# Optimization experiments

Hardware: AMD Instinct MI355X
Metric: run time of the kernel (lower is better)

Reference implementation:

```python
import jax, jax.numpy as jnp
import numpy as np

N_HEAD = 16
R = 4  # reciprocal rank

def setup_inputs() -> dict:
    key = jax.random.key(0)
    ks = jax.random.split(key, 8)
    B, T, C = 2, 2048, 1024
    H = N_HEAD
    D = C // H
    D_std = D - R
    x = jax.random.normal(ks[0], (B, T, C), dtype=jnp.float32)
    W_attn = jax.random.normal(ks[1], (3 * C, C), dtype=jnp.float32) * (1.0 / np.sqrt(C))
    W_proj = jax.random.normal(ks[2], (C, C), dtype=jnp.float32) * (1.0 / np.sqrt(C))
    w_std = jnp.full((H,), D_std / D, dtype=jnp.float32)
    w_rec = jnp.full((H,), R / D, dtype=jnp.float32)
    skip_std = jnp.float32(2.0)
    skip_low = jnp.float32(-3.0)
    rwr_alpha = jnp.full((H,), 0.05, dtype=jnp.float32)
    return {"x": x, "W_attn": W_attn, "W_proj": W_proj, "w_std": w_std,
            "w_rec": w_rec, "skip_std": skip_std, "skip_low": skip_low,
            "rwr_alpha": rwr_alpha}

def reference(x, W_attn, W_proj, w_std, w_rec, skip_std, skip_low, rwr_alpha):
    B, T, C = x.shape
    H = N_HEAD
    D = C // H
    D_std = D - R
    # fused QKV projection: [Qf | Kf | V]
    fused = jnp.einsum('btc,fc->btf', x, W_attn)
    qf, kf, v = jnp.split(fused, 3, axis=-1)
    Qf = qf.reshape(B, T, H, D).transpose(0, 2, 1, 3)  # (B,H,T,D)
    Kf = kf.reshape(B, T, H, D).transpose(0, 2, 1, 3)
    V = v.reshape(B, T, H, D).transpose(0, 2, 1, 3)
    # dynamic per-head gate scaling folded into Qf/Kf
    g_std = jnp.sqrt(jnp.clip(w_std * jax.nn.sigmoid(skip_std), 1e-8))  # (H,)
    g_rec = jnp.sqrt(jnp.clip(w_rec * jax.nn.sigmoid(skip_low), 1e-8))  # (H,)
    scale = jnp.concatenate([
        jnp.broadcast_to(g_std[:, None], (H, D_std)),
        jnp.broadcast_to(g_rec[:, None], (H, R)),
    ], axis=-1)  # (H, D)
    scale = scale[None, :, None, :]  # (1,H,1,D)
    Qf = Qf * scale
    Kf = Kf * scale
    # causal SDPA (scale = 1/sqrt(head_dim), dropout=0)
    scores = jnp.einsum('bhqd,bhkd->bhqk', Qf, Kf) / jnp.sqrt(jnp.float32(D))
    causal = jnp.tril(jnp.ones((T, T), dtype=bool))
    scores = jnp.where(causal[None, None], scores, jnp.float32(-1e30))
    attn = jax.nn.softmax(scores, axis=-1)
    y = jnp.einsum('bhqk,bhkd->bhqd', attn, V)
    # self-restart mix: out = (1-alpha)*attn_out + alpha*V, alpha in [0, 0.5]
    alpha = jnp.clip(rwr_alpha, 0.0, 0.5)[None, :, None, None]
    y = (1.0 - alpha) * y + alpha * V
    y = y.transpose(0, 2, 1, 3).reshape(B, T, C)
    return jnp.einsum('btc,oc->bto', y, W_proj)
```

## Files before the change

### kernel.cpp

```cpp
#include <hip/hip_runtime.h>
#include <hip/hip_bf16.h>
#include <math.h>
#include <stdint.h>

#define B_    2
#define T_    2048
#define C_    1024
#define H_    16
#define D_    64
#define R_    4
#define DSTD  60
#define F_    3072
#define BT_   (B_ * T_)

typedef __bf16 bf16x8 __attribute__((ext_vector_type(8)));
typedef __bf16 bf16x4 __attribute__((ext_vector_type(4)));
typedef float  f32x4  __attribute__((ext_vector_type(4)));

__device__ __forceinline__ int swz_blk(int row, int blk) {
    return blk ^ ((row >> 1) & 7);
}

__device__ __forceinline__ void gload_lds16(const void* g, void* l) {
    __builtin_amdgcn_global_load_lds(
        (const __attribute__((address_space(1))) uint32_t*)g,
        (__attribute__((address_space(3))) uint32_t*)l, 16, 0, 0);
}

__global__ __launch_bounds__(256) void cast_kernel(
    const float* __restrict__ in, __bf16* __restrict__ outp, int n4)
{
    int i = blockIdx.x * 256 + threadIdx.x;
    if (i < n4) {
        float4 v = ((const float4*)in)[i];
        bf16x4 o;
        o[0] = (__bf16)v.x; o[1] = (__bf16)v.y;
        o[2] = (__bf16)v.z; o[3] = (__bf16)v.w;
        ((bf16x4*)outp)[i] = o;
    }
}

__global__ __launch_bounds__(256) void gemm_qkv_kernel(
    const __bf16* __restrict__ A,
    const __bf16* __restrict__ Bw,
    const float* __restrict__ w_std, const float* __restrict__ w_rec,
    const float* __restrict__ skip_std, const float* __restrict__ skip_low,
    __bf16* __restrict__ Q, __bf16* __restrict__ K, __bf16* __restrict__ V)
{
    __shared__ __bf16 As[128 * 32];
    __shared__ __bf16 Bs[128 * 32];

    const int tid  = threadIdx.x;
    const int row0 = blockIdx.x * 128;
    const int col0 = blockIdx.y * 128;

    const int w    = tid >> 6;
    const int lane = tid & 63;
    const int quad = lane >> 4;
    const int lt   = lane & 15;
    const int wm   = w >> 1;
    const int wn   = w & 1;

    const int lrow = tid >> 2;
    const int lcol = (tid & 3) * 8;

    f32x4 acc[4][4];
#pragma unroll
    for (int i = 0; i < 4; ++i)
#pragma unroll
        for (int j = 0; j < 4; ++j)
#pragma unroll
            for (int r = 0; r < 4; ++r) acc[i][j][r] = 0.f;

    for (int kt = 0; kt < C_ / 32; ++kt) {
        const int k0 = kt * 32;
        __syncthreads();
#pragma unroll
        for (int rr = 0; rr < 2; ++rr) {
            gload_lds16(A  + (size_t)(row0 + rr * 64 + lrow) * C_ + k0 + lcol,
                        As + rr * 2048 + tid * 8);
            gload_lds16(Bw + (size_t)(col0 + rr * 64 + lrow) * C_ + k0 + lcol,
                        Bs + rr * 2048 + tid * 8);
        }
        __syncthreads();

        bf16x8 af[4], bf[4];
#pragma unroll
        for (int i = 0; i < 4; ++i)
            af[i] = *(const bf16x8*)&As[(wm * 64 + i * 16 + lt) * 32 + quad * 8];
#pragma unroll
        for (int j = 0; j < 4; ++j)
            bf[j] = *(const bf16x8*)&Bs[(wn * 64 + j * 16 + lt) * 32 + quad * 8];
#pragma unroll
        for (int i = 0; i < 4; ++i)
#pragma unroll
            for (int j = 0; j < 4; ++j)
                acc[i][j] = __builtin_amdgcn_mfma_f32_16x16x32_bf16(af[i], bf[j], acc[i][j], 0, 0, 0);
    }

    const int colbase = col0 + wn * 64;
    const int which   = colbase >> 10;
    const int h       = (colbase & (C_ - 1)) >> 6;

    const float ss = 1.f / (1.f + __expf(-skip_std[0]));
    const float sl = 1.f / (1.f + __expf(-skip_low[0]));
    const float gs = sqrtf(fmaxf(w_std[h] * ss, 1e-8f));
    const float gr = sqrtf(fmaxf(w_rec[h] * sl, 1e-8f));

    __bf16* dstM = (which == 0) ? Q : (which == 1) ? K : V;

#pragma unroll
    for (int i = 0; i < 4; ++i) {
#pragma unroll
        for (int r = 0; r < 4; ++r) {
            const int row = row0 + wm * 64 + i * 16 + quad * 4 + r;
            const int b = row >> 11;
            const int t = row & (T_ - 1);
            __bf16* dp = dstM + (((size_t)b * H_ + h) * T_ + t) * D_;
#pragma unroll
            for (int j = 0; j < 4; ++j) {
                const int d = j * 16 + lt;
                float val = acc[i][j][r];
                if (which == 0)      val *= ((d < DSTD) ? gs : gr) * 0.125f;
                else if (which == 1) val *= (d < DSTD) ? gs : gr;
                dp[d] = (__bf16)val;
            }
        }
    }
}

__global__ __launch_bounds__(256) void gemm_out_kernel(
    const __bf16* __restrict__ A,
    const __bf16* __restrict__ Bw,
    float* __restrict__ out)
{
    __shared__ __bf16 As[128 * 32];
    __shared__ __bf16 Bs[128 * 32];

    const int tid  = threadIdx.x;
    const int row0 = blockIdx.x * 128;
    const int col0 = blockIdx.y * 128;

    const int w    = tid >> 6;
    const int lane = tid & 63;
    const int quad = lane >> 4;
    const int lt   = lane & 15;
    const int wm   = w >> 1;
    const int wn   = w & 1;

    const int lrow = tid >> 2;
    const int lcol = (tid & 3) * 8;

    f32x4 acc[4][4];
#pragma unroll
    for (int i = 0; i < 4; ++i)
#pragma unroll
        for (int j = 0; j < 4; ++j)
#pragma unroll
            for (int r = 0; r < 4; ++r) acc[i][j][r] = 0.f;

    for (int kt = 0; kt < C_ / 32; ++kt) {
        const int k0 = kt * 32;
        __syncthreads();
#pragma unroll
        for (int rr = 0; rr < 2; ++rr) {
            gload_lds16(A  + (size_t)(row0 + rr * 64 + lrow) * C_ + k0 + lcol,
                        As + rr * 2048 + tid * 8);
            gload_lds16(Bw + (size_t)(col0 + rr * 64 + lrow) * C_ + k0 + lcol,
                        Bs + rr * 2048 + tid * 8);
        }
        __syncthreads();

        bf16x8 af[4], bf[4];
#pragma unroll
        for (int i = 0; i < 4; ++i)
            af[i] = *(const bf16x8*)&As[(wm * 64 + i * 16 + lt) * 32 + quad * 8];
#pragma unroll
        for (int j = 0; j < 4; ++j)
            bf[j] = *(const bf16x8*)&Bs[(wn * 64 + j * 16 + lt) * 32 + quad * 8];
#pragma unroll
        for (int i = 0; i < 4; ++i)
#pragma unroll
            for (int j = 0; j < 4; ++j)
                acc[i][j] = __builtin_amdgcn_mfma_f32_16x16x32_bf16(af[i], bf[j], acc[i][j], 0, 0, 0);
    }

#pragma unroll
    for (int i = 0; i < 4; ++i)
#pragma unroll
        for (int r = 0; r < 4; ++r) {
            const int row = row0 + wm * 64 + i * 16 + quad * 4 + r;
            float* op = out + (size_t)row * C_ + col0 + wn * 64 + lt;
#pragma unroll
            for (int j = 0; j < 4; ++j)
                op[j * 16] = acc[i][j][r];
        }
}

__global__ __launch_bounds__(256) void attn_kernel(
    const __bf16* __restrict__ Q, const __bf16* __restrict__ K,
    const __bf16* __restrict__ V, const float* __restrict__ rwr_alpha,
    __bf16* __restrict__ Y)
{
    __shared__ __align__(16) __bf16 Ks[2][64][72];
    __shared__ __align__(16) __bf16 Vt[2][64][72];
    __shared__ __align__(16) __bf16 Ps[4][16][72];

    const int tid = threadIdx.x;
    const int nqt = T_ / 64;
    const int bh  = blockIdx.x & 31;
    const int qt  = nqt - 1 - (blockIdx.x >> 5);
    const int h   = bh & (H_ - 1);
    const int b   = bh >> 4;

    const __bf16* Qb = Q + (((size_t)b * H_ + h) * T_) * D_;
    const __bf16* Kb = K + (((size_t)b * H_ + h) * T_) * D_;
    const __bf16* Vb = V + (((size_t)b * H_ + h) * T_) * D_;

    const int w    = tid >> 6;
    const int lane = tid & 63;
    const int quad = lane >> 4;
    const int lt   = lane & 15;

    const int sr = tid >> 2;
    const int sc = (tid & 3) * 16;
    const int kb = sr >> 3, ko = sr & 7;

    const __bf16* qrow = Qb + (size_t)(qt * 64 + w * 16 + lt) * D_;
    bf16x8 qf[2];
    qf[0] = *(const bf16x8*)(qrow + quad * 8);
    qf[1] = *(const bf16x8*)(qrow + 32 + quad * 8);

    {
        const __bf16* ks = Kb + sr * 64 + sc;
        const __bf16* vs = Vb + sr * 64 + sc;
        bf16x8 k1 = *(const bf16x8*)(ks);
        bf16x8 k2 = *(const bf16x8*)(ks + 8);
        bf16x8 v1 = *(const bf16x8*)(vs);
        bf16x8 v2 = *(const bf16x8*)(vs + 8);
        *(bf16x8*)&Ks[0][sr][sc]     = k1;
        *(bf16x8*)&Ks[0][sr][sc + 8] = k2;
#pragma unroll
        for (int u = 0; u < 8; ++u) {
            Vt[0][sc + u    ][(kb ^ ((u >> 1) & 7)) * 8 + ko]       = v1[u];
            Vt[0][sc + 8 + u][(kb ^ (((u + 8) >> 1) & 7)) * 8 + ko] = v2[u];
        }
    }
    __syncthreads();

    float m = -1e30f;
    float l[4] = {0.f, 0.f, 0.f, 0.f};
    f32x4 oacc[4];
#pragma unroll
    for (int n = 0; n < 4; ++n)
#pragma unroll
        for (int r = 0; r < 4; ++r) oacc[n][r] = 0.f;

    for (int kt = 0; kt <= qt; ++kt) {
        const int cur = kt & 1;
        const bool pre = (kt < qt);

        bf16x8 k1, k2, v1, v2;
        if (pre) {
            const __bf16* ks = Kb + (size_t)(kt + 1) * 4096 + sr * 64 + sc;
            const __bf16* vs = Vb + (size_t)(kt + 1) * 4096 + sr * 64 + sc;
            k1 = *(const bf16x8*)(ks);
            k2 = *(const bf16x8*)(ks + 8);
            v1 = *(const bf16x8*)(vs);
            v2 = *(const bf16x8*)(vs + 8);
        }

        f32x4 sacc[4];
#pragma unroll
        for (int n = 0; n < 4; ++n)
#pragma unroll
            for (int r = 0; r < 4; ++r) sacc[n][r] = 0.f;
#pragma unroll
        for (int kk = 0; kk < 2; ++kk) {
#pragma unroll
            for (int n = 0; n < 4; ++n) {
                bf16x8 bk = *(const bf16x8*)&Ks[cur][n * 16 + lt][kk * 32 + quad * 8];
                sacc[n] = __builtin_amdgcn_mfma_f32_16x16x32_bf16(qf[kk], bk, sacc[n], 0, 0, 0);
            }
        }

        if (kt == qt) {
            const int lq = w * 16 + quad * 4;
#pragma unroll
            for (int n = 0; n < 4; ++n) {
                const int col = n * 16 + lt;
#pragma unroll
                for (int r = 0; r < 4; ++r)
                    if (col > lq + r) sacc[n][r] = -1e30f;
            }
        }

        float lm = sacc[0][0];
#pragma unroll
        for (int n = 0; n < 4; ++n)
#pragma unroll
            for (int r = 0; r < 4; ++r) lm = fmaxf(lm, sacc[n][r]);
#pragma unroll
        for (int d = 1; d < 64; d <<= 1) lm = fmaxf(lm, __shfl_xor(lm, d));
        const float mn = fmaxf(m, lm);
        {
            int need = (mn > m) ? 1 : 0;
            need = __builtin_amdgcn_readfirstlane(need);
            if (need) {
                const float al = __expf(m - mn);
#pragma unroll
                for (int r = 0; r < 4; ++r) l[r] *= al;
#pragma unroll
                for (int n = 0; n < 4; ++n)
#pragma unroll
                    for (int r = 0; r < 4; ++r) oacc[n][r] *= al;
            }
            m = mn;
        }

#pragma unroll
        for (int r = 0; r < 4; ++r) {
            const int prow = quad * 4 + r;
            float rs = 0.f;
#pragma unroll
            for (int n = 0; n < 4; ++n) {
                const float p = __expf(sacc[n][r] - m);
                rs += p;
                const int col = n * 16 + lt;
                Ps[w][prow][swz_blk(prow, col >> 3) * 8 + (col & 7)] = (__bf16)p;
            }
            rs += __shfl_xor(rs, 1);
            rs += __shfl_xor(rs, 2);
            rs += __shfl_xor(rs, 4);
            rs += __shfl_xor(rs, 8);
            l[r] += rs;
        }

#pragma unroll
        for (int kk = 0; kk < 2; ++kk) {
            bf16x8 ap = *(const bf16x8*)&Ps[w][lt][swz_blk(lt, kk * 4 + quad) * 8];
#pragma unroll
            for (int nd = 0; nd < 4; ++nd) {
                const int drow = nd * 16 + lt;
                bf16x8 bv = *(const bf16x8*)&Vt[cur][drow][swz_blk(drow, kk * 4 + quad) * 8];
                oacc[nd] = __builtin_amdgcn_mfma_f32_16x16x32_bf16(ap, bv, oacc[nd], 0, 0, 0);
            }
        }

        if (pre) {
            const int nxt = 1 - cur;
            *(bf16x8*)&Ks[nxt][sr][sc]     = k1;
            *(bf16x8*)&Ks[nxt][sr][sc + 8] = k2;
#pragma unroll
            for (int u = 0; u < 8; ++u) {
                Vt[nxt][sc + u    ][(kb ^ ((u >> 1) & 7)) * 8 + ko]       = v1[u];
                Vt[nxt][sc + 8 + u][(kb ^ (((u + 8) >> 1) & 7)) * 8 + ko] = v2[u];
            }
        }
        __syncthreads();
    }

    const float a = fminf(fmaxf(rwr_alpha[h], 0.f), 0.5f);
#pragma unroll
    for (int r = 0; r < 4; ++r) {
        const float inv = 1.f / l[r];
        const int qg = qt * 64 + w * 16 + quad * 4 + r;
        const __bf16* vp = Vb + (size_t)qg * D_;
        __bf16* yp = Y + ((size_t)(b * T_ + qg)) * C_ + h * D_;
#pragma unroll
        for (int nd = 0; nd < 4; ++nd) {
            const int d = nd * 16 + lt;
            yp[d] = (__bf16)((1.f - a) * oacc[nd][r] * inv + a * (float)vp[d]);
        }
    }
}

extern "C" void kernel_launch(void* const* d_in, const int* in_sizes, int n_in,
                              void* d_out, int out_size, void* d_ws, size_t ws_size,
                              hipStream_t stream) {
    const float* x        = (const float*)d_in[0];
    const float* W_attn   = (const float*)d_in[1];
    const float* W_proj   = (const float*)d_in[2];
    const float* w_std    = (const float*)d_in[3];
    const float* w_rec    = (const float*)d_in[4];
    const float* skip_std = (const float*)d_in[5];
    const float* skip_low = (const float*)d_in[6];
    const float* rwr      = (const float*)d_in[7];
    float* out = (float*)d_out;

    const size_t nX  = (size_t)BT_ * C_;
    const size_t nWa = (size_t)F_ * C_;
    const size_t nWp = (size_t)C_ * C_;
    const size_t per = (size_t)B_ * H_ * T_ * D_;

    __bf16* xb  = (__bf16*)d_ws;
    __bf16* Wab = xb  + nX;
    __bf16* Wpb = Wab + nWa;
    __bf16* Qb  = Wpb + nWp;
    __bf16* Kb  = Qb  + per;
    __bf16* Vb  = Kb  + per;
    __bf16* Yb  = Vb  + per;

    cast_kernel<<<dim3((nX  / 4 + 255) / 256), 256, 0, stream>>>(x,      xb,  nX  / 4);
    cast_kernel<<<dim3((nWa / 4 + 255) / 256), 256, 0, stream>>>(W_attn, Wab, nWa / 4);
    cast_kernel<<<dim3((nWp / 4 + 255) / 256), 256, 0, stream>>>(W_proj, Wpb, nWp / 4);

    gemm_qkv_kernel<<<dim3(BT_ / 128, F_ / 128), 256, 0, stream>>>(
        xb, Wab, w_std, w_rec, skip_std, skip_low, Qb, Kb, Vb);
    attn_kernel<<<dim3(32 * (T_ / 64)), 256, 0, stream>>>(Qb, Kb, Vb, rwr, Yb);
    gemm_out_kernel<<<dim3(BT_ / 128, C_ / 128), 256, 0, stream>>>(Yb, Wpb, out);
}
```

Measured before the change: 212.7 us.

## Fuse cast launches, swizzle unpadded attention LDS tiles, defer row-sum reduction

Merges the three fp32-to-bf16 cast launches into one kernel that dispatches by index range, removing two launch overheads. In attention, drops the LDS padding, applies an XOR swizzle to the K and V tiles, and rearranges the K/V staging so each thread loads two adjacent key rows. This lets the transposed V stores be written as packed 32-bit pairs instead of single bf16 values. The per-tile softmax row-sum shuffle reduction is moved out of the loop and done once at the end, trading some per-lane accumulation for fewer cross-lane shuffles in the hot loop.

```diff
diff --git a/kernel.cpp b/kernel.cpp
--- a/kernel.cpp
+++ b/kernel.cpp
@@ -17,8 +17,14 @@
 typedef __bf16 bf16x4 __attribute__((ext_vector_type(4)));
 typedef float  f32x4  __attribute__((ext_vector_type(4)));
 
-__device__ __forceinline__ int swz_blk(int row, int blk) {
+__device__ __forceinline__ int swz(int row, int blk) {
     return blk ^ ((row >> 1) & 7);
+}
+
+__device__ __forceinline__ void st_pair(__bf16* p, __bf16 a, __bf16 b) {
+    union { __bf16 h[2]; uint32_t u; } t;
+    t.h[0] = a; t.h[1] = b;
+    *(uint32_t*)p = t.u;
 }
 
 __device__ __forceinline__ void gload_lds16(const void* g, void* l) {
@@ -27,17 +33,29 @@
         (__attribute__((address_space(3))) uint32_t*)l, 16, 0, 0);
 }
 
-__global__ __launch_bounds__(256) void cast_kernel(
-    const float* __restrict__ in, __bf16* __restrict__ outp, int n4)
+__global__ __launch_bounds__(256) void cast3_kernel(
+    const float* __restrict__ a, int na4,
+    const float* __restrict__ b, int nb4,
+    const float* __restrict__ c, int nc4,
+    __bf16* __restrict__ oa, __bf16* __restrict__ ob, __bf16* __restrict__ oc)
 {
     int i = blockIdx.x * 256 + threadIdx.x;
-    if (i < n4) {
-        float4 v = ((const float4*)in)[i];
-        bf16x4 o;
-        o[0] = (__bf16)v.x; o[1] = (__bf16)v.y;
-        o[2] = (__bf16)v.z; o[3] = (__bf16)v.w;
-        ((bf16x4*)outp)[i] = o;
-    }
+    const float* s; __bf16* d; int j = i;
+    if (j < na4) { s = a; d = oa; }
+    else {
+        j -= na4;
+        if (j < nb4) { s = b; d = ob; }
+        else {
+            j -= nb4;
+            if (j >= nc4) return;
+            s = c; d = oc;
+        }
+    }
+    float4 v = ((const float4*)s)[j];
+    bf16x4 o;
+    o[0] = (__bf16)v.x; o[1] = (__bf16)v.y;
+    o[2] = (__bf16)v.z; o[3] = (__bf16)v.w;
+    ((bf16x4*)d)[j] = o;
 }
 
 __global__ __launch_bounds__(256) void gemm_qkv_kernel(
@@ -202,9 +220,9 @@
     const __bf16* __restrict__ V, const float* __restrict__ rwr_alpha,
     __bf16* __restrict__ Y)
 {
-    __shared__ __align__(16) __bf16 Ks[2][64][72];
-    __shared__ __align__(16) __bf16 Vt[2][64][72];
-    __shared__ __align__(16) __bf16 Ps[4][16][72];
+    __shared__ __align__(16) __bf16 Ks[2][64][64];
+    __shared__ __align__(16) __bf16 Vt[2][64][64];
+    __shared__ __align__(16) __bf16 Ps[4][16][64];
 
     const int tid = threadIdx.x;
     const int nqt = T_ / 64;
@@ -222,9 +240,9 @@
     const int quad = lane >> 4;
     const int lt   = lane & 15;
 
-    const int sr = tid >> 2;
-    const int sc = (tid & 3) * 16;
-    const int kb = sr >> 3, ko = sr & 7;
+    const int kp = (tid >> 3) * 2;
+    const int dc = (tid & 7) * 8;
+    const int kblk = kp >> 3, koff = kp & 7;
 
     const __bf16* qrow = Qb + (size_t)(qt * 64 + w * 16 + lt) * D_;
     bf16x8 qf[2];
@@ -232,18 +250,18 @@
     qf[1] = *(const bf16x8*)(qrow + 32 + quad * 8);
 
     {
-        const __bf16* ks = Kb + sr * 64 + sc;
-        const __bf16* vs = Vb + sr * 64 + sc;
+        const __bf16* ks = Kb + (size_t)kp * 64 + dc;
+        const __bf16* vs = Vb + (size_t)kp * 64 + dc;
         bf16x8 k1 = *(const bf16x8*)(ks);
-        bf16x8 k2 = *(const bf16x8*)(ks + 8);
+        bf16x8 k2 = *(const bf16x8*)(ks + 64);
         bf16x8 v1 = *(const bf16x8*)(vs);
-        bf16x8 v2 = *(const bf16x8*)(vs + 8);
-        *(bf16x8*)&Ks[0][sr][sc]     = k1;
-        *(bf16x8*)&Ks[0][sr][sc + 8] = k2;
+        bf16x8 v2 = *(const bf16x8*)(vs + 64);
+        *(bf16x8*)&Ks[0][kp    ][swz(kp, dc >> 3) * 8] = k1;
+        *(bf16x8*)&Ks[0][kp + 1][swz(kp, dc >> 3) * 8] = k2;
 #pragma unroll
         for (int u = 0; u < 8; ++u) {
-            Vt[0][sc + u    ][(kb ^ ((u >> 1) & 7)) * 8 + ko]       = v1[u];
-            Vt[0][sc + 8 + u][(kb ^ (((u + 8) >> 1) & 7)) * 8 + ko] = v2[u];
+            const int row = dc + u;
+            st_pair(&Vt[0][row][swz(row, kblk) * 8 + koff], v1[u], v2[u]);
         }
     }
     __syncthreads();
@@ -262,12 +280,12 @@
 
         bf16x8 k1, k2, v1, v2;
         if (pre) {
-            const __bf16* ks = Kb + (size_t)(kt + 1) * 4096 + sr * 64 + sc;
-            const __bf16* vs = Vb + (size_t)(kt + 1) * 4096 + sr * 64 + sc;
+            const __bf16* ks = Kb + (size_t)(kt + 1) * 4096 + (size_t)kp * 64 + dc;
+            const __bf16* vs = Vb + (size_t)(kt + 1) * 4096 + (size_t)kp * 64 + dc;
             k1 = *(const bf16x8*)(ks);
-            k2 = *(const bf16x8*)(ks + 8);
+            k2 = *(const bf16x8*)(ks + 64);
             v1 = *(const bf16x8*)(vs);
-            v2 = *(const bf16x8*)(vs + 8);
+            v2 = *(const bf16x8*)(vs + 64);
         }
 
         f32x4 sacc[4];
@@ -279,7 +297,8 @@
         for (int kk = 0; kk < 2; ++kk) {
 #pragma unroll
             for (int n = 0; n < 4; ++n) {
-                bf16x8 bk = *(const bf16x8*)&Ks[cur][n * 16 + lt][kk * 32 + quad * 8];
+                const int row = n * 16 + lt;
+                bf16x8 bk = *(const bf16x8*)&Ks[cur][row][swz(row, kk * 4 + quad) * 8];
                 sacc[n] = __builtin_amdgcn_mfma_f32_16x16x32_bf16(qf[kk], bk, sacc[n], 0, 0, 0);
             }
         }
@@ -321,40 +340,33 @@
 #pragma unroll
         for (int r = 0; r < 4; ++r) {
             const int prow = quad * 4 + r;
-            float rs = 0.f;
 #pragma unroll
             for (int n = 0; n < 4; ++n) {
                 const float p = __expf(sacc[n][r] - m);
-                rs += p;
-                const int col = n * 16 + lt;
-                Ps[w][prow][swz_blk(prow, col >> 3) * 8 + (col & 7)] = (__bf16)p;
-            }
-            rs += __shfl_xor(rs, 1);
-            rs += __shfl_xor(rs, 2);
-            rs += __shfl_xor(rs, 4);
-            rs += __shfl_xor(rs, 8);
-            l[r] += rs;
+                l[r] += p;
+                Ps[w][prow][swz(prow, n * 2 + (lt >> 3)) * 8 + (lt & 7)] = (__bf16)p;
+            }
         }
 
 #pragma unroll
         for (int kk = 0; kk < 2; ++kk) {
-            bf16x8 ap = *(const bf16x8*)&Ps[w][lt][swz_blk(lt, kk * 4 + quad) * 8];
+            bf16x8 ap = *(const bf16x8*)&Ps[w][lt][swz(lt, kk * 4 + quad) * 8];
 #pragma unroll
             for (int nd = 0; nd < 4; ++nd) {
                 const int drow = nd * 16 + lt;
-                bf16x8 bv = *(const bf16x8*)&Vt[cur][drow][swz_blk(drow, kk * 4 + quad) * 8];
+                bf16x8 bv = *(const bf16x8*)&Vt[cur][drow][swz(drow, kk * 4 + quad) * 8];
                 oacc[nd] = __builtin_amdgcn_mfma_f32_16x16x32_bf16(ap, bv, oacc[nd], 0, 0, 0);
             }
         }
 
         if (pre) {
             const int nxt = 1 - cur;
-            *(bf16x8*)&Ks[nxt][sr][sc]     = k1;
-            *(bf16x8*)&Ks[nxt][sr][sc + 8] = k2;
+            *(bf16x8*)&Ks[nxt][kp    ][swz(kp, dc >> 3) * 8] = k1;
+            *(bf16x8*)&Ks[nxt][kp + 1][swz(kp, dc >> 3) * 8] = k2;
 #pragma unroll
             for (int u = 0; u < 8; ++u) {
-                Vt[nxt][sc + u    ][(kb ^ ((u >> 1) & 7)) * 8 + ko]       = v1[u];
-                Vt[nxt][sc + 8 + u][(kb ^ (((u + 8) >> 1) & 7)) * 8 + ko] = v2[u];
+                const int row = dc + u;
+                st_pair(&Vt[nxt][row][swz(row, kblk) * 8 + koff], v1[u], v2[u]);
             }
         }
         __syncthreads();
@@ -363,7 +375,12 @@
     const float a = fminf(fmaxf(rwr_alpha[h], 0.f), 0.5f);
 #pragma unroll
     for (int r = 0; r < 4; ++r) {
-        const float inv = 1.f / l[r];
+        float lr = l[r];
+        lr += __shfl_xor(lr, 1);
+        lr += __shfl_xor(lr, 2);
+        lr += __shfl_xor(lr, 4);
+        lr += __shfl_xor(lr, 8);
+        const float inv = 1.f / lr;
         const int qg = qt * 64 + w * 16 + quad * 4 + r;
         const __bf16* vp = Vb + (size_t)qg * D_;
         __bf16* yp = Y + ((size_t)(b * T_ + qg)) * C_ + h * D_;
@@ -401,9 +418,9 @@
     __bf16* Vb  = Kb  + per;
     __bf16* Yb  = Vb  + per;
 
-    cast_kernel<<<dim3((nX  / 4 + 255) / 256), 256, 0, stream>>>(x,      xb,  nX  / 4);
-    cast_kernel<<<dim3((nWa / 4 + 255) / 256), 256, 0, stream>>>(W_attn, Wab, nWa / 4);
-    cast_kernel<<<dim3((nWp / 4 + 255) / 256), 256, 0, stream>>>(W_proj, Wpb, nWp / 4);
+    const int na4 = nX / 4, nb4 = nWa / 4, nc4 = nWp / 4;
+    cast3_kernel<<<dim3((na4 + nb4 + nc4 + 255) / 256), 256, 0, stream>>>(
+        x, na4, W_attn, nb4, W_proj, nc4, xb, Wab, Wpb);
 
     gemm_qkv_kernel<<<dim3(BT_ / 128, F_ / 128), 256, 0, stream>>>(
         xb, Wab, w_std, w_rec, skip_std, skip_low, Qb, Kb, Vb);
```

Result: faster. 195.0 us (-8.3%).
